# Performance work log

Measured on AMD Instinct MI355X. Metric: run time of the kernel, lower is better.

Reference implementation:

```python
import jax, jax.numpy as jnp
import numpy as np

TRIM_RATIO = 0.1
B, N, D_IN, D_H, N_OUT, D_OUT = 64, 1024, 512, 1024, 10, 1


def setup_inputs() -> dict:
    key = jax.random.key(0)
    ks = jax.random.split(key, 10)
    X = jax.random.normal(ks[0], (B, N, D_IN), dtype=jnp.float32)
    # ragged valid lengths in [N//2, N]; guarantees num_valid > 2*k for trim_ratio=0.1
    lengths = jax.random.randint(ks[1], (B,), N // 2, N + 1)
    mask = (jnp.arange(N)[None, :] < lengths[:, None]).astype(jnp.float32)
    s_in, s_h = 1.0 / np.sqrt(D_IN), 1.0 / np.sqrt(D_H)
    W1 = jax.random.uniform(ks[2], (D_IN, D_H), jnp.float32, -s_in, s_in)
    b1 = jax.random.uniform(ks[3], (D_H,), jnp.float32, -s_in, s_in)
    W2 = jax.random.uniform(ks[4], (D_H, D_H), jnp.float32, -s_h, s_h)
    b2 = jax.random.uniform(ks[5], (D_H,), jnp.float32, -s_h, s_h)
    W3 = jax.random.uniform(ks[6], (D_H, D_H), jnp.float32, -s_h, s_h)
    b3 = jax.random.uniform(ks[7], (D_H,), jnp.float32, -s_h, s_h)
    W4 = jax.random.uniform(ks[8], (D_H, N_OUT * D_OUT), jnp.float32, -s_h, s_h)
    b4 = jax.random.uniform(ks[9], (N_OUT * D_OUT,), jnp.float32, -s_h, s_h)
    return {"X": X, "mask": mask, "W1": W1, "b1": b1, "W2": W2, "b2": b2,
            "W3": W3, "b3": b3, "W4": W4, "b4": b4}


def reference(X, mask, W1, b1, W2, b2, W3, b3, W4, b4):
    # encode MLP: [B,N,D_IN] -> [B,N,D_H]
    encoded = jax.nn.relu(jnp.einsum('bni,ih->bnh', X, W1) + b1) @ W2 + b2
    masked = encoded * mask[..., None]
    num_valid = mask.sum(axis=-1).astype(jnp.int32)                 # [B]
    k = (num_valid.astype(jnp.float32) * TRIM_RATIO).astype(jnp.int32)  # floor, as int()
    # push invalid rows to +inf so valid elements occupy the first num_valid slots after sort
    padded = jnp.where(mask[..., None] > 0, masked, jnp.inf)
    sorted_v = jnp.sort(padded, axis=1)                             # per-column sort, [B,N,D_H]
    pos = jnp.arange(N)[None, :]
    keep = (pos >= k[:, None]) & (pos < (num_valid - k)[:, None])   # [B,N]
    summed = jnp.sum(jnp.where(keep[..., None], sorted_v, 0.0), axis=1)  # [B,D_H]
    denom = (num_valid - 2 * k).astype(jnp.float32)[:, None]
    aggregated = summed / denom                                     # trimmed mean
    # decode MLP
    out = jax.nn.relu(aggregated @ W3 + b3) @ W4 + b4               # [B, N_OUT*D_OUT]
    out = out.reshape(-1, N_OUT, D_OUT).squeeze(-1)                 # [B, N_OUT]
    return out
```

## Files before the change

kernel.cpp:

```cpp
#include <hip/hip_runtime.h>


typedef _Float16 half8  __attribute__((ext_vector_type(8)));
typedef _Float16 half4v __attribute__((ext_vector_type(4)));
typedef float    floatx4 __attribute__((ext_vector_type(4)));
typedef unsigned long long ull2 __attribute__((ext_vector_type(2)));

#define GLD_LDS(g, l)                                                                     \
  __builtin_amdgcn_global_load_lds((const __attribute__((address_space(1))) void*)(g),    \
                                   (__attribute__((address_space(3))) void*)(l), 16, 0, 0)

__global__ void prep_nv(const float* __restrict__ mask, int* __restrict__ nv_arr,
                        int* __restrict__ k_arr) {
  int b = blockIdx.x, lane = threadIdx.x;
  const float4* mp = (const float4*)(mask + (b << 10));
  float s = 0.f;
#pragma unroll
  for (int i = 0; i < 4; ++i) {
    float4 v = mp[lane + i * 64];
    s += v.x + v.y + v.z + v.w;
  }
#pragma unroll
  for (int off = 32; off > 0; off >>= 1) s += __shfl_xor(s, off, 64);
  if (lane == 0) {
    int nv = (int)(s + 0.5f);
    int kk = (int)((float)nv * 0.1f);
    nv_arr[b] = nv;
    k_arr[b] = kk;
  }
}

__global__ void conv_x(const float* __restrict__ X, _Float16* __restrict__ X16) {
  int i = (blockIdx.x * 256 + threadIdx.x) * 8;
  float4 a = *(const float4*)(X + i);
  float4 c = *(const float4*)(X + i + 4);
  half8 h;
  h[0] = (_Float16)a.x; h[1] = (_Float16)a.y; h[2] = (_Float16)a.z; h[3] = (_Float16)a.w;
  h[4] = (_Float16)c.x; h[5] = (_Float16)c.y; h[6] = (_Float16)c.z; h[7] = (_Float16)c.w;
  *(half8*)(X16 + i) = h;
}

__global__ void transpose_conv(const float* __restrict__ W, _Float16* __restrict__ WT,
                               int R, int C) {
  __shared__ _Float16 tile[64][65];
  int r0 = blockIdx.x * 64, c0 = blockIdx.y * 64;
  for (int i = threadIdx.x; i < 4096; i += 256) {
    int r = i >> 6, c = i & 63;
    tile[r][c] = (_Float16)W[(size_t)(r0 + r) * C + c0 + c];
  }
  __syncthreads();
  for (int i = threadIdx.x; i < 4096; i += 256) {
    int c = i >> 6, r = i & 63;
    WT[(size_t)(c0 + c) * R + r0 + r] = tile[r][c];
  }
}

template <int KDIM, int MODE>
__global__ __launch_bounds__(256, 3) void gemm_kernel(
    const _Float16* __restrict__ Aop, const _Float16* __restrict__ Bop,
    const float* __restrict__ bias, const int* __restrict__ nv_arr,
    _Float16* __restrict__ outp) {
  __shared__ __align__(16) _Float16 ldsA[128 * 64];
  __shared__ __align__(16) _Float16 ldsB[128 * 64];
  int i0, j0;
  int bid = blockIdx.x;
  if (MODE == 1) {
    i0 = (bid & 7) * 128; j0 = (bid >> 3) * 128;
    if ((j0 & 1023) >= nv_arr[j0 >> 10]) return;
  } else {
    i0 = (bid >> 3) * 128; j0 = (bid & 7) * 128;
    if ((i0 & 1023) >= nv_arr[i0 >> 10]) return;
  }
  const int t = threadIdx.x, lane = t & 63;
  const int wv = t >> 6, wi = wv & 1, wj = wv >> 1;
  const int lr = lane & 15, q = lane >> 4;

  floatx4 acc[4][4] = {};

  const int gch = (t & 7) ^ ((t >> 3) & 7);
  const _Float16* gA[4];
  const _Float16* gB[4];
  _Float16* lA[4];
  _Float16* lB[4];
#pragma unroll
  for (int r = 0; r < 4; ++r) {
    int row = r * 32 + (t >> 3);
    gA[r] = Aop + (size_t)(i0 + row) * KDIM + gch * 8;
    gB[r] = Bop + (size_t)(j0 + row) * KDIM + gch * 8;
    lA[r] = ldsA + (r * 256 + (t & ~63)) * 8;
    lB[r] = ldsB + (r * 256 + (t & ~63)) * 8;
  }

  int aoff[4], boff[4];
#pragma unroll
  for (int mi = 0; mi < 4; ++mi) {
    int row = wi * 64 + mi * 16 + lr;
    aoff[mi] = row * 64 + ((q ^ (row & 7)) * 8);
  }
#pragma unroll
  for (int nj = 0; nj < 4; ++nj) {
    int row = wj * 64 + nj * 16 + lr;
    boff[nj] = row * 64 + ((q ^ (row & 7)) * 8);
  }

  for (int kt = 0; kt < KDIM / 64; ++kt) {
#pragma unroll
    for (int r = 0; r < 4; ++r) GLD_LDS(gA[r], lA[r]);
#pragma unroll
    for (int r = 0; r < 4; ++r) GLD_LDS(gB[r], lB[r]);
#pragma unroll
    for (int r = 0; r < 4; ++r) { gA[r] += 64; gB[r] += 64; }
    __syncthreads();
#pragma unroll
    for (int kk = 0; kk < 2; ++kk) {
      half8 af[4], bf[4];
#pragma unroll
      for (int mi = 0; mi < 4; ++mi) af[mi] = *(const half8*)&ldsA[aoff[mi] ^ (kk * 32)];
#pragma unroll
      for (int nj = 0; nj < 4; ++nj) bf[nj] = *(const half8*)&ldsB[boff[nj] ^ (kk * 32)];
#pragma unroll
      for (int mi = 0; mi < 4; ++mi)
#pragma unroll
        for (int nj = 0; nj < 4; ++nj)
          acc[mi][nj] =
              __builtin_amdgcn_mfma_f32_16x16x32_f16(af[mi], bf[nj], acc[mi][nj], 0, 0, 0);
    }
    __syncthreads();
  }

  if (MODE == 1) {
#pragma unroll
    for (int mi = 0; mi < 4; ++mi) {
      int ih = i0 + wi * 64 + mi * 16 + q * 4;
      floatx4 bb = *(const floatx4*)&bias[ih];
#pragma unroll
      for (int nj = 0; nj < 4; ++nj) {
        int j = j0 + wj * 64 + nj * 16 + lr;
        floatx4 v = acc[mi][nj];
        half4v hv;
#pragma unroll
        for (int r = 0; r < 4; ++r) hv[r] = (_Float16)fmaxf(v[r] + bb[r], 0.f);
        *(half4v*)&outp[(size_t)j * 1024 + ih] = hv;
      }
    }
  } else {
#pragma unroll
    for (int nj = 0; nj < 4; ++nj) {
      int j = j0 + wj * 64 + nj * 16 + lr;
      float bj = bias[j];
#pragma unroll
      for (int mi = 0; mi < 4; ++mi) {
        int im = i0 + wi * 64 + mi * 16 + q * 4;
        int bb = im >> 10, n = im & 1023;
        floatx4 v = acc[mi][nj];
        half4v hv;
#pragma unroll
        for (int r = 0; r < 4; ++r) hv[r] = (_Float16)(v[r] + bj);
        *(half4v*)&outp[((size_t)bb << 20) + ((size_t)j << 10) + (size_t)n] = hv;
      }
    }
  }
}

#define NB 1024
__global__ __launch_bounds__(256) void trim_kernel(const _Float16* __restrict__ encT,
                                                   const int* __restrict__ nv_arr,
                                                   const int* __restrict__ k_arr,
                                                   float* __restrict__ agg) {
  __shared__ unsigned long long hist[4 * NB];
  int t = threadIdx.x, lane = t & 63, w = t >> 6;
  int blk = blockIdx.x;
  int batch = blk >> 8;
  int h = ((blk & 255) << 2) + w;
  unsigned long long* hw = hist + w * NB;

  {
    ull2 z = {0ull, 0ull};
    ull2* hp = (ull2*)hw;
#pragma unroll
    for (int i = 0; i < 8; ++i) hp[lane * 8 + (i ^ (lane & 7))] = z;
  }

  int nv = nv_arr[batch], kk = k_arr[batch];
  const _Float16* col = encT + ((size_t)batch << 20) + ((size_t)h << 10);
  const uint4* p = (const uint4*)col + lane * 2;
  uint4 u0 = p[0], u1 = p[1];
  unsigned vals[8] = {u0.x, u0.y, u0.z, u0.w, u1.x, u1.y, u1.z, u1.w};
  int nvalid = nv - lane * 16;

#pragma unroll
  for (int d = 0; d < 8; ++d) {
    unsigned u = vals[d];
#pragma unroll
    for (int sub = 0; sub < 2; ++sub) {
      int idx = d * 2 + sub;
      if (idx < nvalid) {
        unsigned short bits = (unsigned short)(sub ? (u >> 16) : (u & 0xffffu));
        _Float16 hvv;
        __builtin_memcpy(&hvv, &bits, 2);
        float v = (float)hvv;
        v = fminf(fmaxf(v, -8.0f), 7.999f);
        int fx = (int)((v + 8.0f) * 4096.0f + 0.5f);
        int bin = fx >> 6;
        int eb = bin ^ (((bin >> 4) & 7) << 1);
        atomicAdd(&hw[eb], (1ull << 48) | (unsigned long long)(unsigned)fx);
      }
    }
  }

  ull2 bb[8];
  {
    ull2* hp = (ull2*)hw;
#pragma unroll
    for (int i = 0; i < 8; ++i) bb[i] = hp[lane * 8 + (i ^ (lane & 7))];
  }
  int c[16];
  float sf[16];
  int ct = 0;
  float st = 0.f;
#pragma unroll
  for (int i = 0; i < 16; ++i) {
    unsigned long long u = bb[i >> 1][i & 1];
    int cc = (int)(u >> 48);
    float ss = (float)(unsigned)(u & 0xffffffffu) * (1.0f / 4096.0f) - 8.0f * (float)cc;
    c[i] = cc;
    sf[i] = ss;
    ct += cc;
    st += ss;
  }
  int ci = ct;
  float si = st;
#pragma unroll
  for (int off = 1; off < 64; off <<= 1) {
    int cu = __shfl_up(ci, off, 64);
    float su = __shfl_up(si, off, 64);
    if (lane >= off) { ci += cu; si += su; }
  }
  int cex = ci - ct;
  float sex = si - st;
  int r1 = kk, r2 = nv - kk;
  float S1 = 0.f, S2 = 0.f;
#pragma unroll
  for (int i = 0; i < 16; ++i) {
    int cc = c[i];
    float ss = sf[i];
    if (cc > 0) {
      float mu = ss / (float)cc;
      if (cex < r1 && r1 <= cex + cc) S1 = sex + (float)(r1 - cex) * mu;
      if (cex < r2 && r2 <= cex + cc) S2 = sex + (float)(r2 - cex) * mu;
    }
    cex += cc;
    sex += ss;
  }
#pragma unroll
  for (int off = 32; off > 0; off >>= 1) {
    S1 += __shfl_xor(S1, off, 64);
    S2 += __shfl_xor(S2, off, 64);
  }
  if (lane == 0) {
    float denom = (float)(nv - 2 * kk);
    agg[(batch << 10) + h] = (S2 - S1) / denom;
  }
}

__global__ void decode1(const float* __restrict__ agg, const float* __restrict__ W3,
                        const float* __restrict__ b3, float* __restrict__ A3) {
  __shared__ float al[1024];
  int b = blockIdx.x;
  int h = blockIdx.y * 256 + threadIdx.x;
  for (int i = threadIdx.x; i < 1024; i += 256) al[i] = agg[(b << 10) + i];
  __syncthreads();
  float acc = b3[h];
#pragma unroll 8
  for (int k2 = 0; k2 < 1024; ++k2) acc = fmaf(al[k2], W3[(size_t)k2 * 1024 + h], acc);
  A3[(b << 10) + h] = fmaxf(acc, 0.f);
}

__global__ void decode2(const float* __restrict__ A3, const float* __restrict__ W4,
                        const float* __restrict__ b4, float* __restrict__ outp) {
  __shared__ float red[4][10];
  int b = blockIdx.x, t = threadIdx.x, lane = t & 63, w = t >> 6;
  float part[10];
#pragma unroll
  for (int o = 0; o < 10; ++o) part[o] = 0.f;
#pragma unroll
  for (int jj = 0; jj < 4; ++jj) {
    int h2 = jj * 256 + t;
    float a = A3[(b << 10) + h2];
#pragma unroll
    for (int o = 0; o < 10; ++o) part[o] = fmaf(a, W4[h2 * 10 + o], part[o]);
  }
#pragma unroll
  for (int o = 0; o < 10; ++o)
#pragma unroll
    for (int off = 32; off > 0; off >>= 1) part[o] += __shfl_xor(part[o], off, 64);
  if (lane == 0)
#pragma unroll
    for (int o = 0; o < 10; ++o) red[w][o] = part[o];
  __syncthreads();
  if (t < 10) outp[b * 10 + t] = b4[t] + red[0][t] + red[1][t] + red[2][t] + red[3][t];
}

extern "C" void kernel_launch(void* const* d_in, const int* in_sizes, int n_in,
                              void* d_out, int out_size, void* d_ws, size_t ws_size,
                              hipStream_t stream) {
  const float* X = (const float*)d_in[0];
  const float* mask = (const float*)d_in[1];
  const float* W1 = (const float*)d_in[2];
  const float* b1 = (const float*)d_in[3];
  const float* W2 = (const float*)d_in[4];
  const float* b2 = (const float*)d_in[5];
  const float* W3 = (const float*)d_in[6];
  const float* b3 = (const float*)d_in[7];
  const float* W4 = (const float*)d_in[8];
  const float* b4 = (const float*)d_in[9];
  float* outp = (float*)d_out;
  char* ws = (char*)d_ws;

  _Float16* X16 = (_Float16*)(ws);
  _Float16* H1 = (_Float16*)(ws + 67108864ull);
  _Float16* encT = (_Float16*)(ws + 201326592ull);
  _Float16* W1T = (_Float16*)(ws + 335544320ull);
  _Float16* W2T = (_Float16*)(ws + 336592896ull);
  float* agg = (float*)(ws + 338690048ull);
  float* A3 = (float*)(ws + 338952192ull);
  int* nv_arr = (int*)(ws + 339214336ull);
  int* k_arr = (int*)(ws + 339214592ull);

  prep_nv<<<64, 64, 0, stream>>>(mask, nv_arr, k_arr);
  conv_x<<<16384, 256, 0, stream>>>(X, X16);
  transpose_conv<<<dim3(8, 16), 256, 0, stream>>>(W1, W1T, 512, 1024);
  transpose_conv<<<dim3(16, 16), 256, 0, stream>>>(W2, W2T, 1024, 1024);
  gemm_kernel<512, 1><<<4096, 256, 0, stream>>>(W1T, X16, b1, nv_arr, H1);
  gemm_kernel<1024, 2><<<4096, 256, 0, stream>>>(H1, W2T, b2, nv_arr, encT);
  trim_kernel<<<16384, 256, 0, stream>>>(encT, nv_arr, k_arr, agg);
  decode1<<<dim3(64, 4), 256, 0, stream>>>(agg, W3, b3, A3);
  decode2<<<64, 256, 0, stream>>>(A3, W4, b4, outp);
}
```

Baseline: 613.4 us.

## Use 32-bit count histogram in trim kernel and remap GEMM tile order

The trimmed-mean kernel now keeps only 32-bit per-bin counts in LDS instead of packed 64-bit count+fixed-point-sum atomics. After locating the two boundary bins with a prefix scan, it recomputes the partial sums from register-held values through extra wave reductions. This halves the LDS histogram footprint and replaces 64-bit atomics with 32-bit ones, at the cost of a second reduction pass. Separately, the GEMM block index mapping is reordered so consecutive blocks share the thin operand, aiming at better cache reuse.

```diff
diff --git a/kernel.cpp b/kernel.cpp
--- a/kernel.cpp
+++ b/kernel.cpp
@@ -4,7 +4,6 @@
 typedef _Float16 half8  __attribute__((ext_vector_type(8)));
 typedef _Float16 half4v __attribute__((ext_vector_type(4)));
 typedef float    floatx4 __attribute__((ext_vector_type(4)));
-typedef unsigned long long ull2 __attribute__((ext_vector_type(2)));
 
 #define GLD_LDS(g, l)                                                                     \
   __builtin_amdgcn_global_load_lds((const __attribute__((address_space(1))) void*)(g),    \
@@ -64,11 +63,13 @@
   __shared__ __align__(16) _Float16 ldsB[128 * 64];
   int i0, j0;
   int bid = blockIdx.x;
+  int fat = (((bid >> 6) << 3) | (bid & 7)) * 128;
+  int thin = ((bid >> 3) & 7) * 128;
   if (MODE == 1) {
-    i0 = (bid & 7) * 128; j0 = (bid >> 3) * 128;
+    i0 = thin; j0 = fat;
     if ((j0 & 1023) >= nv_arr[j0 >> 10]) return;
   } else {
-    i0 = (bid >> 3) * 128; j0 = (bid & 7) * 128;
+    i0 = fat; j0 = thin;
     if ((i0 & 1023) >= nv_arr[i0 >> 10]) return;
   }
   const int t = threadIdx.x, lane = t & 63;
@@ -167,18 +168,17 @@
                                                    const int* __restrict__ nv_arr,
                                                    const int* __restrict__ k_arr,
                                                    float* __restrict__ agg) {
-  __shared__ unsigned long long hist[4 * NB];
+  __shared__ unsigned int cnt[4 * NB];
   int t = threadIdx.x, lane = t & 63, w = t >> 6;
   int blk = blockIdx.x;
   int batch = blk >> 8;
   int h = ((blk & 255) << 2) + w;
-  unsigned long long* hw = hist + w * NB;
-
+  unsigned int* cw = cnt + w * NB;
+  uint4* cp = (uint4*)cw;
   {
-    ull2 z = {0ull, 0ull};
-    ull2* hp = (ull2*)hw;
-#pragma unroll
-    for (int i = 0; i < 8; ++i) hp[lane * 8 + (i ^ (lane & 7))] = z;
+    uint4 z = {0u, 0u, 0u, 0u};
+#pragma unroll
+    for (int i = 0; i < 4; ++i) cp[lane * 4 + (i ^ ((lane >> 1) & 3))] = z;
   }
 
   int nv = nv_arr[batch], kk = k_arr[batch];
@@ -188,78 +188,101 @@
   unsigned vals[8] = {u0.x, u0.y, u0.z, u0.w, u1.x, u1.y, u1.z, u1.w};
   int nvalid = nv - lane * 16;
 
+  float vv[16];
+  int bn[16];
 #pragma unroll
   for (int d = 0; d < 8; ++d) {
     unsigned u = vals[d];
 #pragma unroll
     for (int sub = 0; sub < 2; ++sub) {
       int idx = d * 2 + sub;
+      unsigned short bits = (unsigned short)(sub ? (u >> 16) : (u & 0xffffu));
+      _Float16 hvv;
+      __builtin_memcpy(&hvv, &bits, 2);
+      float v = (float)hvv;
       if (idx < nvalid) {
-        unsigned short bits = (unsigned short)(sub ? (u >> 16) : (u & 0xffffu));
-        _Float16 hvv;
-        __builtin_memcpy(&hvv, &bits, 2);
-        float v = (float)hvv;
         v = fminf(fmaxf(v, -8.0f), 7.999f);
-        int fx = (int)((v + 8.0f) * 4096.0f + 0.5f);
-        int bin = fx >> 6;
-        int eb = bin ^ (((bin >> 4) & 7) << 1);
-        atomicAdd(&hw[eb], (1ull << 48) | (unsigned long long)(unsigned)fx);
+        int bin = (int)((v + 8.0f) * 64.0f);
+        bin = min(NB - 1, bin);
+        vv[idx] = v;
+        bn[idx] = bin;
+        int Lb = bin >> 4, jc = (bin >> 2) & 3;
+        int phys = ((Lb << 2) + (jc ^ ((Lb >> 1) & 3))) * 4 + (bin & 3);
+        atomicAdd(&cw[phys], 1u);
+      } else {
+        vv[idx] = 0.f;
+        bn[idx] = -1;
       }
     }
   }
 
-  ull2 bb[8];
+  int c[16];
   {
-    ull2* hp = (ull2*)hw;
-#pragma unroll
-    for (int i = 0; i < 8; ++i) bb[i] = hp[lane * 8 + (i ^ (lane & 7))];
-  }
-  int c[16];
-  float sf[16];
+    uint4 rb[4];
+#pragma unroll
+    for (int i = 0; i < 4; ++i) rb[i] = cp[lane * 4 + (i ^ ((lane >> 1) & 3))];
+#pragma unroll
+    for (int i = 0; i < 4; ++i) {
+      c[4 * i] = (int)rb[i].x; c[4 * i + 1] = (int)rb[i].y;
+      c[4 * i + 2] = (int)rb[i].z; c[4 * i + 3] = (int)rb[i].w;
+    }
+  }
   int ct = 0;
-  float st = 0.f;
-#pragma unroll
-  for (int i = 0; i < 16; ++i) {
-    unsigned long long u = bb[i >> 1][i & 1];
-    int cc = (int)(u >> 48);
-    float ss = (float)(unsigned)(u & 0xffffffffu) * (1.0f / 4096.0f) - 8.0f * (float)cc;
-    c[i] = cc;
-    sf[i] = ss;
-    ct += cc;
-    st += ss;
-  }
+#pragma unroll
+  for (int i = 0; i < 16; ++i) ct += c[i];
   int ci = ct;
-  float si = st;
 #pragma unroll
   for (int off = 1; off < 64; off <<= 1) {
     int cu = __shfl_up(ci, off, 64);
-    float su = __shfl_up(si, off, 64);
-    if (lane >= off) { ci += cu; si += su; }
+    if (lane >= off) ci += cu;
   }
   int cex = ci - ct;
-  float sex = si - st;
   int r1 = kk, r2 = nv - kk;
-  float S1 = 0.f, S2 = 0.f;
+  int p1 = -1, p2 = -1;
+  {
+    int run = cex;
+#pragma unroll
+    for (int i = 0; i < 16; ++i) {
+      int cc = c[i];
+      if (run < r1 && r1 <= run + cc) p1 = ((lane * 16 + i) << 12) | run;
+      if (run < r2 && r2 <= run + cc) p2 = ((lane * 16 + i) << 12) | run;
+      run += cc;
+    }
+  }
+#pragma unroll
+  for (int off = 32; off > 0; off >>= 1) {
+    p1 = max(p1, __shfl_xor(p1, off, 64));
+    p2 = max(p2, __shfl_xor(p2, off, 64));
+  }
+  int b1 = p1 >> 12, cex1 = p1 & 4095;
+  int b2 = p2 >> 12, cex2 = p2 & 4095;
+  float s1 = 0.f, s2 = 0.f, tm = 0.f;
+  int c1 = 0, c2 = 0;
 #pragma unroll
   for (int i = 0; i < 16; ++i) {
-    int cc = c[i];
-    float ss = sf[i];
-    if (cc > 0) {
-      float mu = ss / (float)cc;
-      if (cex < r1 && r1 <= cex + cc) S1 = sex + (float)(r1 - cex) * mu;
-      if (cex < r2 && r2 <= cex + cc) S2 = sex + (float)(r2 - cex) * mu;
-    }
-    cex += cc;
-    sex += ss;
+    int b = bn[i];
+    float v = vv[i];
+    if (b == b1) { s1 += v; c1++; }
+    if (b == b2) { s2 += v; c2++; }
+    if (b > b1 && b < b2) tm += v;
   }
 #pragma unroll
   for (int off = 32; off > 0; off >>= 1) {
-    S1 += __shfl_xor(S1, off, 64);
-    S2 += __shfl_xor(S2, off, 64);
+    s1 += __shfl_xor(s1, off, 64);
+    s2 += __shfl_xor(s2, off, 64);
+    tm += __shfl_xor(tm, off, 64);
+    c1 += __shfl_xor(c1, off, 64);
+    c2 += __shfl_xor(c2, off, 64);
+  }
+  float mid;
+  if (b1 == b2) {
+    mid = (float)(r2 - r1) * (s1 / (float)c1);
+  } else {
+    mid = (float)(cex1 + c1 - r1) * (s1 / (float)c1) + tm +
+          (float)(r2 - cex2) * (s2 / (float)c2);
   }
   if (lane == 0) {
-    float denom = (float)(nv - 2 * kk);
-    agg[(batch << 10) + h] = (S2 - S1) / denom;
+    agg[(batch << 10) + h] = mid / (float)(nv - 2 * kk);
   }
 }
 
```

Result: faster. 582.8 us (-5.0%).
